# Kernel optimization log

Hardware: AMD Instinct MI355X
Metric: run time of the kernel (lower is better)

The kernel has to match this reference:

```python
import jax, jax.numpy as jnp
import numpy as np

NT, NGRID, NX, HID, NY = 365, 1000, 20, 256, 1


def setup_inputs() -> dict:
    key = jax.random.key(0)
    ks = jax.random.split(key, 10)
    s_in = 1.0 / np.sqrt(NX)
    s_h = 1.0 / np.sqrt(HID)
    inp = {
        "x": jax.random.normal(ks[0], (NT, NGRID, NX), dtype=jnp.float32),
        "wt_ih": jnp.zeros((4 * HID, HID), dtype=jnp.float32),
        "W_in": jax.random.uniform(ks[1], (HID, NX), jnp.float32, -s_in, s_in),
        "b_in": jax.random.uniform(ks[2], (HID,), jnp.float32, -s_in, s_in),
        "W_ih": jax.random.uniform(ks[3], (4 * HID, HID), jnp.float32, -s_h, s_h),
        "W_hh": jax.random.uniform(ks[4], (4 * HID, HID), jnp.float32, -s_h, s_h),
        "b_ih": jax.random.uniform(ks[5], (4 * HID,), jnp.float32, -s_h, s_h),
        "b_hh": jax.random.uniform(ks[6], (4 * HID,), jnp.float32, -s_h, s_h),
        "W_out": jax.random.uniform(ks[7], (NY, HID), jnp.float32, -s_h, s_h),
        "b_out": jax.random.uniform(ks[8], (NY,), jnp.float32, -s_h, s_h),
    }
    return inp


def _lstm_forward(x, W_in, b_in, W_ih, W_hh, b_ih, b_hh, W_out, b_out):
    # linearIn + ReLU: [nt, ngrid, hid]
    x0 = jax.nn.relu(jnp.einsum("tnx,hx->tnh", x, W_in) + b_in)
    # precompute input contribution to gates for all timesteps: [nt, ngrid, 4*hid]
    gx = jnp.einsum("tnh,gh->tng", x0, W_ih) + b_ih + b_hh
    h0 = jnp.zeros((x.shape[1], HID), dtype=x.dtype)
    c0 = jnp.zeros((x.shape[1], HID), dtype=x.dtype)

    def step(carry, gx_t):
        h, c = carry
        gates = gx_t + h @ W_hh.T  # [ngrid, 4*hid]
        i, f, g, o = jnp.split(gates, 4, axis=-1)  # torch LSTMCell gate order
        i = jax.nn.sigmoid(i)
        f = jax.nn.sigmoid(f)
        g = jnp.tanh(g)
        o = jax.nn.sigmoid(o)
        c_new = f * c + i * g
        h_new = o * jnp.tanh(c_new)
        return (h_new, c_new), h_new

    _, hs = jax.lax.scan(step, (h0, c0), gx)  # hs: [nt, ngrid, hid]
    return jnp.einsum("tnh,yh->tny", hs, W_out) + b_out


def reference(x, wt_ih, W_in, b_in, W_ih, W_hh, b_ih, b_hh, W_out, b_out):
    # wt_ih only perturbs weights in training mode (and is zero here); eval-mode math:
    return _lstm_forward(x, W_in, b_in, W_ih, W_hh, b_ih, b_hh, W_out, b_out)
```

## Files before the change

### kernel.cpp

```cpp
#include <hip/hip_runtime.h>
#include <hip/hip_fp16.h>

#define NT    365
#define NGRID 1000
#define NXI   20
#define HID   256
#define GATES 1024
#define MROWS 365000
#define MBLK  5704
#define MPAD  (MBLK * 64)
#define NCL   63
#define CPTS  16
#define HX_TOT ((size_t)NT * NCL * 1024)
#define HX_ZERO ((size_t)NCL * 1024)

typedef _Float16 half8 __attribute__((ext_vector_type(8)));
typedef float floatx4 __attribute__((ext_vector_type(4)));
typedef unsigned long long u64;

#define SENT 0xFFFFFFFFFFFFFFFFull

__device__ _Float16 g_gx[(size_t)MPAD * GATES];
__device__ _Float16 g_wif[64 * 8 * 512];
__device__ _Float16 g_whf[2 * 32 * 8 * 64 * 8];
__device__ u64 g_hx[HX_TOT];

__device__ __forceinline__ float fsig(float x) {
  return __fdividef(1.f, 1.f + __expf(-x));
}
__device__ __forceinline__ float ftanh(float x) {
  return 1.f - __fdividef(2.f, __expf(2.f * x) + 1.f);
}

__global__ __launch_bounds__(256) void init_kernel(float* __restrict__ y) {
  const size_t i = (size_t)blockIdx.x * 256 + threadIdx.x;
  const size_t j = i * 2;
  if (j < HX_TOT)     g_hx[j]     = (j < HX_ZERO)     ? 0ull : SENT;
  if (j + 1 < HX_TOT) g_hx[j + 1] = (j + 1 < HX_ZERO) ? 0ull : SENT;
  if (i < MROWS) y[i] = 0.f;
}

__global__ __launch_bounds__(256) void pack_wf_kernel(
    const float* __restrict__ W_ih, const float* __restrict__ W_hh) {
  const int gid = blockIdx.x * 256 + threadIdx.x;
  const float* src;
  _Float16* dst;
  int n, k0, lane;
  if (gid < 32768) {
    const int tile = gid >> 9;
    const int ks   = (gid >> 6) & 7;
    lane = gid & 63;
    n  = tile * 16 + (lane & 15);
    k0 = ks * 32 + (lane >> 4) * 8;
    src = W_ih + n * HID + k0;
    dst = g_wif + ((size_t)(tile * 8 + ks) * 64 + lane) * 8;
  } else {
    const int rem = gid - 32768;
    const int b2  = rem >> 14;
    const int lt  = (rem >> 9) & 31;
    const int ks  = (rem >> 6) & 7;
    lane = rem & 63;
    const int nt = (lt >> 3) * 16 + b2 * 8 + (lt & 7);
    n  = nt * 16 + (lane & 15);
    k0 = ks * 32 + (lane >> 4) * 8;
    src = W_hh + n * HID + k0;
    dst = g_whf + ((size_t)((b2 * 32 + lt) * 8 + ks) * 64 + lane) * 8;
  }
  const float4 a = *(const float4*)(src);
  const float4 b = *(const float4*)(src + 4);
  half8 h;
  h[0] = (_Float16)a.x; h[1] = (_Float16)a.y; h[2] = (_Float16)a.z; h[3] = (_Float16)a.w;
  h[4] = (_Float16)b.x; h[5] = (_Float16)b.y; h[6] = (_Float16)b.z; h[7] = (_Float16)b.w;
  *(half8*)dst = h;
}

__global__ __launch_bounds__(256, 2) void gx_kernel(
    const float* __restrict__ x, const float* __restrict__ W_in,
    const float* __restrict__ b_in, const float* __restrict__ b_ih,
    const float* __restrict__ b_hh) {
  __shared__ float s_x[64 * NXI];
  __shared__ _Float16 s_x0[64 * 264];
  __shared__ _Float16 s_out[64 * 264];

  const int tid  = threadIdx.x;
  const int lane = tid & 63;
  const int w    = tid >> 6;
  const int m0   = blockIdx.x * 64;

  #pragma unroll
  for (int i = 0; i < 5; ++i) {
    const int idx = i * 256 + tid;
    size_t g = (size_t)m0 * NXI + idx;
    const size_t gmax = (size_t)MROWS * NXI - 1;
    if (g > gmax) g = gmax;
    s_x[idx] = x[g];
  }
  float wv[NXI];
  #pragma unroll
  for (int k = 0; k < NXI; ++k) wv[k] = W_in[tid * NXI + k];
  const float bv = b_in[tid];
  __syncthreads();

  for (int r = 0; r < 64; ++r) {
    float acc = bv;
    #pragma unroll
    for (int qq = 0; qq < 5; ++qq) {
      const float4 xa = *(const float4*)&s_x[r * NXI + qq * 4];
      acc += xa.x * wv[qq * 4 + 0] + xa.y * wv[qq * 4 + 1] +
             xa.z * wv[qq * 4 + 2] + xa.w * wv[qq * 4 + 3];
    }
    s_x0[r * 264 + tid] = (_Float16)fmaxf(acc, 0.f);
  }
  __syncthreads();

  for (int ng = 0; ng < 4; ++ng) {
    floatx4 acc[4][4];
    #pragma unroll
    for (int mi = 0; mi < 4; ++mi)
      #pragma unroll
      for (int ni = 0; ni < 4; ++ni) acc[mi][ni] = (floatx4){0.f, 0.f, 0.f, 0.f};

    #pragma unroll
    for (int ks = 0; ks < 8; ++ks) {
      half8 a[4], bfr[4];
      #pragma unroll
      for (int mi = 0; mi < 4; ++mi)
        a[mi] = *(const half8*)&s_x0[(mi * 16 + (lane & 15)) * 264 + ks * 32 + (lane >> 4) * 8];
      #pragma unroll
      for (int ni = 0; ni < 4; ++ni) {
        const int nt = ng * 16 + w * 4 + ni;
        bfr[ni] = *(const half8*)(g_wif + ((size_t)(nt * 8 + ks) * 64 + lane) * 8);
      }
      #pragma unroll
      for (int mi = 0; mi < 4; ++mi)
        #pragma unroll
        for (int ni = 0; ni < 4; ++ni)
          acc[mi][ni] = __builtin_amdgcn_mfma_f32_16x16x32_f16(a[mi], bfr[ni], acc[mi][ni], 0, 0, 0);
    }

    #pragma unroll
    for (int ni = 0; ni < 4; ++ni) {
      const int g = ng * 256 + (w * 4 + ni) * 16 + (lane & 15);
      const float bias = b_ih[g] + b_hh[g];
      const int colw = (w * 4 + ni) * 16 + (lane & 15);
      #pragma unroll
      for (int mi = 0; mi < 4; ++mi)
        #pragma unroll
        for (int r = 0; r < 4; ++r)
          s_out[(mi * 16 + (lane >> 4) * 4 + r) * 264 + colw] = (_Float16)(acc[mi][ni][r] + bias);
    }
    __syncthreads();

    #pragma unroll
    for (int i = 0; i < 8; ++i) {
      const int cid = i * 256 + tid;
      const int row = cid >> 5;
      const int c8  = (cid & 31) * 8;
      const half8 v = *(const half8*)&s_out[row * 264 + c8];
      const int phi = ((c8 >> 7) & 1) * 512 + ng * 128 + (c8 & 127);
      *(half8*)(g_gx + (size_t)(m0 + row) * GATES + phi) = v;
    }
    __syncthreads();
  }
}

__global__ __launch_bounds__(256, 1) void rec_kernel(
    const float* __restrict__ W_out, const float* __restrict__ b_out,
    float* __restrict__ y) {
  __shared__ float s_g[4 * 16 * 132];
  __shared__ u64   s_h[2][1024];

  const int tid = threadIdx.x;
  const int l   = tid & 63;
  const int w   = tid >> 6;
  const int c   = blockIdx.x >> 1;
  const int b   = blockIdx.x & 1;
  const int pt  = l & 15;
  const int jg  = l >> 4;

  half8 wf[8][8];
  #pragma unroll
  for (int slot = 0; slot < 8; ++slot) {
    const int lt = (slot >> 1) * 8 + 2 * w + (slot & 1);
    #pragma unroll
    for (int kk = 0; kk < 4; ++kk) {
      wf[slot][kk] = *(const half8*)(g_whf +
          ((size_t)((b * 32 + lt) * 8 + (b * 4 + kk)) * 64 + l) * 8);
      wf[slot][4 + kk] = *(const half8*)(g_whf +
          ((size_t)((b * 32 + lt) * 8 + ((1 - b) * 4 + kk)) * 64 + l) * 8);
    }
  }

  float cs[8];
  float wo[8];
  #pragma unroll
  for (int j = 0; j < 8; ++j) {
    cs[j] = 0.f;
    wo[j] = W_out[b * 128 + 32 * w + jg * 8 + j];
  }
  const float bo_eff = (b == 0 && w == 0) ? b_out[0] : 0.f;
  const int n_pt  = c * CPTS + pt;
  const int rn_pt = (n_pt < NGRID) ? n_pt : (NGRID - 1);
  const int peer0 = (1 - b) * 4;

  for (int i = tid; i < 1024; i += 256) s_h[0][i] = 0ull;
  __syncthreads();

  for (int t = 0; t < NT; ++t) {
    const int cur = t & 1, nxt = cur ^ 1;

    half8 gxr[4];
    {
      const _Float16* gsrc = g_gx + ((size_t)t * NGRID + rn_pt) * GATES
                           + b * 512 + 32 * w + jg * 8;
      #pragma unroll
      for (int off = 0; off < 4; ++off)
        gxr[off] = *(const half8*)(gsrc + off * 128);
    }

    const u64* hsrc = g_hx + ((size_t)t * NCL + c) * 1024;
    u64 pv[8];
    #pragma unroll
    for (int kk = 0; kk < 4; ++kk) {
      pv[2 * kk]     = __hip_atomic_load(hsrc +       (peer0 + kk) * 64 + l,
                                         __ATOMIC_RELAXED, __HIP_MEMORY_SCOPE_AGENT);
      pv[2 * kk + 1] = __hip_atomic_load(hsrc + 512 + (peer0 + kk) * 64 + l,
                                         __ATOMIC_RELAXED, __HIP_MEMORY_SCOPE_AGENT);
    }

    floatx4 acc[8];
    #pragma unroll
    for (int i = 0; i < 8; ++i) acc[i] = (floatx4){0.f, 0.f, 0.f, 0.f};

    #pragma unroll
    for (int kk = 0; kk < 4; ++kk) {
      union { u64 u[2]; half8 h; } af;
      af.u[0] = s_h[cur][kk * 64 + l];
      af.u[1] = s_h[cur][512 + kk * 64 + l];
      #pragma unroll
      for (int i = 0; i < 8; ++i)
        acc[i] = __builtin_amdgcn_mfma_f32_16x16x32_f16(af.h, wf[i][kk], acc[i], 0, 0, 0);
    }

    {
      bool pending = false;
      #pragma unroll
      for (int k = 0; k < 8; ++k) pending |= (pv[k] == SENT);
      int tries = 0;
      while (pending && ++tries < (1 << 18)) {
        pending = false;
        #pragma unroll
        for (int kk = 0; kk < 4; ++kk) {
          if (pv[2 * kk] == SENT)
            pv[2 * kk] = __hip_atomic_load(hsrc + (peer0 + kk) * 64 + l,
                                           __ATOMIC_RELAXED, __HIP_MEMORY_SCOPE_AGENT);
          if (pv[2 * kk + 1] == SENT)
            pv[2 * kk + 1] = __hip_atomic_load(hsrc + 512 + (peer0 + kk) * 64 + l,
                                               __ATOMIC_RELAXED, __HIP_MEMORY_SCOPE_AGENT);
        }
        #pragma unroll
        for (int k = 0; k < 8; ++k) pending |= (pv[k] == SENT);
      }
    }

    #pragma unroll
    for (int kk = 0; kk < 4; ++kk) {
      union { u64 u[2]; half8 h; } af;
      af.u[0] = pv[2 * kk];
      af.u[1] = pv[2 * kk + 1];
      #pragma unroll
      for (int i = 0; i < 8; ++i)
        acc[i] = __builtin_amdgcn_mfma_f32_16x16x32_f16(af.h, wf[i][4 + kk], acc[i], 0, 0, 0);
    }

    #pragma unroll
    for (int slot = 0; slot < 8; ++slot) {
      const int colw = (slot >> 1) * 32 + (slot & 1) * 16 + pt;
      #pragma unroll
      for (int r = 0; r < 4; ++r)
        s_g[w * 2112 + (jg * 4 + r) * 132 + colw] = acc[slot][r];
    }

    {
      const float* gp = &s_g[w * 2112 + pt * 132 + jg * 8];
      union { u64 u[2]; _Float16 h[8]; } pub;
      float yp = 0.f;
      #pragma unroll
      for (int j = 0; j < 8; ++j) {
        const float gi = gp[j]      + (float)gxr[0][j];
        const float gf = gp[32 + j] + (float)gxr[1][j];
        const float gg = gp[64 + j] + (float)gxr[2][j];
        const float go = gp[96 + j] + (float)gxr[3][j];
        const float i_ = fsig(gi);
        const float f_ = fsig(gf);
        const float g_ = ftanh(gg);
        const float o_ = fsig(go);
        cs[j] = f_ * cs[j] + i_ * g_;
        const float h = o_ * ftanh(cs[j]);
        pub.h[j] = (_Float16)h;
        yp += wo[j] * h;
      }
      if (t < NT - 1) {
        u64* dst = g_hx + ((size_t)(t + 1) * NCL + c) * 1024 + (b * 4 + w) * 64 + l;
        __hip_atomic_store(dst,       pub.u[0], __ATOMIC_RELAXED, __HIP_MEMORY_SCOPE_AGENT);
        __hip_atomic_store(dst + 512, pub.u[1], __ATOMIC_RELAXED, __HIP_MEMORY_SCOPE_AGENT);
      }
      s_h[nxt][w * 64 + l]       = pub.u[0];
      s_h[nxt][512 + w * 64 + l] = pub.u[1];
      yp += __shfl_xor(yp, 16);
      yp += __shfl_xor(yp, 32);
      if (jg == 0 && n_pt < NGRID)
        atomicAdd(&y[(size_t)t * NGRID + n_pt], yp + bo_eff);
    }
    __syncthreads();
  }
}

extern "C" void kernel_launch(void* const* d_in, const int* in_sizes, int n_in,
                              void* d_out, int out_size, void* d_ws, size_t ws_size,
                              hipStream_t stream) {
  (void)in_sizes; (void)n_in; (void)out_size; (void)d_ws; (void)ws_size;
  const float* x     = (const float*)d_in[0];
  const float* W_in  = (const float*)d_in[2];
  const float* b_in  = (const float*)d_in[3];
  const float* W_ih  = (const float*)d_in[4];
  const float* W_hh  = (const float*)d_in[5];
  const float* b_ih  = (const float*)d_in[6];
  const float* b_hh  = (const float*)d_in[7];
  const float* W_out = (const float*)d_in[8];
  const float* b_out = (const float*)d_in[9];
  float* y           = (float*)d_out;

  const int init_blocks = (int)((HX_TOT / 2 + 255) / 256);
  hipLaunchKernelGGL(init_kernel, dim3(init_blocks), dim3(256), 0, stream, y);
  hipLaunchKernelGGL(pack_wf_kernel, dim3(256), dim3(256), 0, stream, W_ih, W_hh);
  hipLaunchKernelGGL(gx_kernel, dim3(MBLK), dim3(256), 0, stream,
                     x, W_in, b_in, b_ih, b_hh);
  hipLaunchKernelGGL(rec_kernel, dim3(NCL * 2), dim3(256), 0, stream, W_out, b_out, y);
}
```

Measured before the change: 1.866 ms.

## Prefetch next-step peer h, fold init into gx kernel, lighten barrier

The recurrent kernel now issues the atomic loads of the peer block's hidden state for step t+1 one iteration early, so that latency overlaps with the current step's MFMA and gate work. The init kernel is folded into gx_kernel, which removes one launch. The gx loads become nontemporal, shared h is stored as half8, and the full __syncthreads is replaced by an LDS-only waitcnt plus s_barrier so outstanding global ops are not drained. Prefetched values may still be the sentinel, in which case the existing spin loop reloads them, at the cost of extra registers.

Result: slower. 2.262 ms (+21.3%).

```diff
diff --git a/kernel.cpp b/kernel.cpp
--- a/kernel.cpp
+++ b/kernel.cpp
@@ -30,14 +30,6 @@
 }
 __device__ __forceinline__ float ftanh(float x) {
   return 1.f - __fdividef(2.f, __expf(2.f * x) + 1.f);
-}
-
-__global__ __launch_bounds__(256) void init_kernel(float* __restrict__ y) {
-  const size_t i = (size_t)blockIdx.x * 256 + threadIdx.x;
-  const size_t j = i * 2;
-  if (j < HX_TOT)     g_hx[j]     = (j < HX_ZERO)     ? 0ull : SENT;
-  if (j + 1 < HX_TOT) g_hx[j + 1] = (j + 1 < HX_ZERO) ? 0ull : SENT;
-  if (i < MROWS) y[i] = 0.f;
 }
 
 __global__ __launch_bounds__(256) void pack_wf_kernel(
@@ -77,7 +69,15 @@
 __global__ __launch_bounds__(256, 2) void gx_kernel(
     const float* __restrict__ x, const float* __restrict__ W_in,
     const float* __restrict__ b_in, const float* __restrict__ b_ih,
-    const float* __restrict__ b_hh) {
+    const float* __restrict__ b_hh, float* __restrict__ y) {
+  {
+    const size_t gid = (size_t)blockIdx.x * 256 + threadIdx.x;
+    const size_t TT  = (size_t)MBLK * 256;
+    for (size_t j = gid; j < HX_TOT; j += TT)
+      g_hx[j] = (j < HX_ZERO) ? 0ull : SENT;
+    if (gid < MROWS) y[gid] = 0.f;
+  }
+
   __shared__ float s_x[64 * NXI];
   __shared__ _Float16 s_x0[64 * 264];
   __shared__ _Float16 s_out[64 * 264];
@@ -168,7 +168,7 @@
     const float* __restrict__ W_out, const float* __restrict__ b_out,
     float* __restrict__ y) {
   __shared__ float s_g[4 * 16 * 132];
-  __shared__ u64   s_h[2][1024];
+  __shared__ half8 s_h[2][256];
 
   const int tid = threadIdx.x;
   const int l   = tid & 63;
@@ -203,11 +203,25 @@
   const int rn_pt = (n_pt < NGRID) ? n_pt : (NGRID - 1);
   const int peer0 = (1 - b) * 4;
 
-  for (int i = tid; i < 1024; i += 256) s_h[0][i] = 0ull;
+  ((u64*)&s_h[0][0])[tid]       = 0ull;
+  ((u64*)&s_h[0][0])[256 + tid] = 0ull;
+
+  u64 pv[8];
+  {
+    const u64* h0 = g_hx + (size_t)c * 1024;
+    #pragma unroll
+    for (int kk = 0; kk < 4; ++kk) {
+      pv[2 * kk]     = __hip_atomic_load(h0 +       (peer0 + kk) * 64 + l,
+                                         __ATOMIC_RELAXED, __HIP_MEMORY_SCOPE_AGENT);
+      pv[2 * kk + 1] = __hip_atomic_load(h0 + 512 + (peer0 + kk) * 64 + l,
+                                         __ATOMIC_RELAXED, __HIP_MEMORY_SCOPE_AGENT);
+    }
+  }
   __syncthreads();
 
   for (int t = 0; t < NT; ++t) {
     const int cur = t & 1, nxt = cur ^ 1;
+    const bool hasnext = (t + 1 < NT);
 
     half8 gxr[4];
     {
@@ -215,34 +229,35 @@
                            + b * 512 + 32 * w + jg * 8;
       #pragma unroll
       for (int off = 0; off < 4; ++off)
-        gxr[off] = *(const half8*)(gsrc + off * 128);
-    }
-
-    const u64* hsrc = g_hx + ((size_t)t * NCL + c) * 1024;
-    u64 pv[8];
+        gxr[off] = __builtin_nontemporal_load((const half8*)(gsrc + off * 128));
+    }
+
+    u64 pf[8];
+    if (hasnext) {
+      const u64* hnxt = g_hx + ((size_t)(t + 1) * NCL + c) * 1024;
+      #pragma unroll
+      for (int kk = 0; kk < 4; ++kk) {
+        pf[2 * kk]     = __hip_atomic_load(hnxt +       (peer0 + kk) * 64 + l,
+                                           __ATOMIC_RELAXED, __HIP_MEMORY_SCOPE_AGENT);
+        pf[2 * kk + 1] = __hip_atomic_load(hnxt + 512 + (peer0 + kk) * 64 + l,
+                                           __ATOMIC_RELAXED, __HIP_MEMORY_SCOPE_AGENT);
+      }
+    }
+
+    floatx4 acc[8];
+    #pragma unroll
+    for (int i = 0; i < 8; ++i) acc[i] = (floatx4){0.f, 0.f, 0.f, 0.f};
+
     #pragma unroll
     for (int kk = 0; kk < 4; ++kk) {
-      pv[2 * kk]     = __hip_atomic_load(hsrc +       (peer0 + kk) * 64 + l,
-                                         __ATOMIC_RELAXED, __HIP_MEMORY_SCOPE_AGENT);
-      pv[2 * kk + 1] = __hip_atomic_load(hsrc + 512 + (peer0 + kk) * 64 + l,
-                                         __ATOMIC_RELAXED, __HIP_MEMORY_SCOPE_AGENT);
-    }
-
-    floatx4 acc[8];
-    #pragma unroll
-    for (int i = 0; i < 8; ++i) acc[i] = (floatx4){0.f, 0.f, 0.f, 0.f};
-
-    #pragma unroll
-    for (int kk = 0; kk < 4; ++kk) {
-      union { u64 u[2]; half8 h; } af;
-      af.u[0] = s_h[cur][kk * 64 + l];
-      af.u[1] = s_h[cur][512 + kk * 64 + l];
+      const half8 af = s_h[cur][kk * 64 + l];
       #pragma unroll
       for (int i = 0; i < 8; ++i)
-        acc[i] = __builtin_amdgcn_mfma_f32_16x16x32_f16(af.h, wf[i][kk], acc[i], 0, 0, 0);
+        acc[i] = __builtin_amdgcn_mfma_f32_16x16x32_f16(af, wf[i][kk], acc[i], 0, 0, 0);
     }
 
     {
+      const u64* hsrc = g_hx + ((size_t)t * NCL + c) * 1024;
       bool pending = false;
       #pragma unroll
       for (int k = 0; k < 8; ++k) pending |= (pv[k] == SENT);
@@ -283,7 +298,7 @@
 
     {
       const float* gp = &s_g[w * 2112 + pt * 132 + jg * 8];
-      union { u64 u[2]; _Float16 h[8]; } pub;
+      union { u64 u[2]; half8 h8; _Float16 h[8]; } pub;
       float yp = 0.f;
       #pragma unroll
       for (int j = 0; j < 8; ++j) {
@@ -300,19 +315,25 @@
         pub.h[j] = (_Float16)h;
         yp += wo[j] * h;
       }
-      if (t < NT - 1) {
+      if (hasnext) {
         u64* dst = g_hx + ((size_t)(t + 1) * NCL + c) * 1024 + (b * 4 + w) * 64 + l;
         __hip_atomic_store(dst,       pub.u[0], __ATOMIC_RELAXED, __HIP_MEMORY_SCOPE_AGENT);
         __hip_atomic_store(dst + 512, pub.u[1], __ATOMIC_RELAXED, __HIP_MEMORY_SCOPE_AGENT);
       }
-      s_h[nxt][w * 64 + l]       = pub.u[0];
-      s_h[nxt][512 + w * 64 + l] = pub.u[1];
+      s_h[nxt][w * 64 + l] = pub.h8;
       yp += __shfl_xor(yp, 16);
       yp += __shfl_xor(yp, 32);
       if (jg == 0 && n_pt < NGRID)
         atomicAdd(&y[(size_t)t * NGRID + n_pt], yp + bo_eff);
     }
-    __syncthreads();
+
+    if (hasnext) {
+      #pragma unroll
+      for (int k = 0; k < 8; ++k) pv[k] = pf[k];
+    }
+
+    asm volatile("s_waitcnt lgkmcnt(0)" ::: "memory");
+    __builtin_amdgcn_s_barrier();
   }
 }
 
@@ -331,10 +352,8 @@
   const float* b_out = (const float*)d_in[9];
   float* y           = (float*)d_out;
 
-  const int init_blocks = (int)((HX_TOT / 2 + 255) / 256);
-  hipLaunchKernelGGL(init_kernel, dim3(init_blocks), dim3(256), 0, stream, y);
   hipLaunchKernelGGL(pack_wf_kernel, dim3(256), dim3(256), 0, stream, W_ih, W_hh);
   hipLaunchKernelGGL(gx_kernel, dim3(MBLK), dim3(256), 0, stream,
-                     x, W_in, b_in, b_ih, b_hh);
+                     x, W_in, b_in, b_ih, b_hh, y);
   hipLaunchKernelGGL(rec_kernel, dim3(NCL * 2), dim3(256), 0, stream, W_out, b_out, y);
 }
```

## Replace per-step atomicAdd output reduction with LDS sum and cross-block flag exchange

Applied to the files above, without the earlier changes.

Instead of every wave atomically adding its partial output projection into y each timestep, the partials are reduced in shared memory per block. The odd-b block publishes its sum through a sentinel-initialized global slot, and the even-b block polls for it two steps later and writes the final y value with a plain store. This removes eight global atomics per grid point per step and the y zero-init, but adds a delayed spin-wait on the critical recurrent loop and extra shared-memory traffic.

Measured after the change: 1.924 ms. +3.1%, slower.

```diff
diff --git a/kernel.cpp b/kernel.cpp
--- a/kernel.cpp
+++ b/kernel.cpp
@@ -13,6 +13,7 @@
 #define CPTS  16
 #define HX_TOT ((size_t)NT * NCL * 1024)
 #define HX_ZERO ((size_t)NCL * 1024)
+#define YX_TOT ((size_t)NT * NCL * 16)
 
 typedef _Float16 half8 __attribute__((ext_vector_type(8)));
 typedef float floatx4 __attribute__((ext_vector_type(4)));
@@ -24,6 +25,7 @@
 __device__ _Float16 g_wif[64 * 8 * 512];
 __device__ _Float16 g_whf[2 * 32 * 8 * 64 * 8];
 __device__ u64 g_hx[HX_TOT];
+__device__ u64 g_yx[YX_TOT];
 
 __device__ __forceinline__ float fsig(float x) {
   return __fdividef(1.f, 1.f + __expf(-x));
@@ -32,12 +34,12 @@
   return 1.f - __fdividef(2.f, __expf(2.f * x) + 1.f);
 }
 
-__global__ __launch_bounds__(256) void init_kernel(float* __restrict__ y) {
+__global__ __launch_bounds__(256) void init_kernel() {
   const size_t i = (size_t)blockIdx.x * 256 + threadIdx.x;
   const size_t j = i * 2;
   if (j < HX_TOT)     g_hx[j]     = (j < HX_ZERO)     ? 0ull : SENT;
   if (j + 1 < HX_TOT) g_hx[j + 1] = (j + 1 < HX_ZERO) ? 0ull : SENT;
-  if (i < MROWS) y[i] = 0.f;
+  if (i < YX_TOT) g_yx[i] = SENT;
 }
 
 __global__ __launch_bounds__(256) void pack_wf_kernel(
@@ -169,6 +171,7 @@
     float* __restrict__ y) {
   __shared__ float s_g[4 * 16 * 132];
   __shared__ u64   s_h[2][1024];
+  __shared__ float s_y[2][4][16];
 
   const int tid = threadIdx.x;
   const int l   = tid & 63;
@@ -198,16 +201,32 @@
     cs[j] = 0.f;
     wo[j] = W_out[b * 128 + 32 * w + jg * 8 + j];
   }
-  const float bo_eff = (b == 0 && w == 0) ? b_out[0] : 0.f;
+  const float bo = b_out[0];
   const int n_pt  = c * CPTS + pt;
   const int rn_pt = (n_pt < NGRID) ? n_pt : (NGRID - 1);
   const int peer0 = (1 - b) * 4;
+  const bool ylane = (w == 0) && (jg == 0);
+  float yo = 0.f;
 
   for (int i = tid; i < 1024; i += 256) s_h[0][i] = 0ull;
   __syncthreads();
 
   for (int t = 0; t < NT; ++t) {
     const int cur = t & 1, nxt = cur ^ 1;
+
+    float own4 = 0.f;
+    u64 ypk = 0;
+    if (ylane && t >= 1) {
+      own4 = s_y[nxt][0][pt] + s_y[nxt][1][pt] +
+             s_y[nxt][2][pt] + s_y[nxt][3][pt];
+      if (b)
+        __hip_atomic_store(&g_yx[((size_t)(t - 1) * NCL + c) * 16 + pt],
+                           (u64)__float_as_uint(own4),
+                           __ATOMIC_RELAXED, __HIP_MEMORY_SCOPE_AGENT);
+    }
+    if (ylane && !b && t >= 2)
+      ypk = __hip_atomic_load(&g_yx[((size_t)(t - 2) * NCL + c) * 16 + pt],
+                              __ATOMIC_RELAXED, __HIP_MEMORY_SCOPE_AGENT);
 
     half8 gxr[4];
     {
@@ -280,6 +299,17 @@
       for (int r = 0; r < 4; ++r)
         s_g[w * 2112 + (jg * 4 + r) * 132 + colw] = acc[slot][r];
     }
+
+    if (ylane && !b && t >= 2) {
+      int ytr = 0;
+      while (ypk == SENT && ++ytr < (1 << 18))
+        ypk = __hip_atomic_load(&g_yx[((size_t)(t - 2) * NCL + c) * 16 + pt],
+                                __ATOMIC_RELAXED, __HIP_MEMORY_SCOPE_AGENT);
+      if (n_pt < NGRID)
+        y[(size_t)(t - 2) * NGRID + n_pt] =
+            yo + __uint_as_float((unsigned)ypk) + bo;
+    }
+    if (ylane && !b && t >= 1) yo = own4;
 
     {
       const float* gp = &s_g[w * 2112 + pt * 132 + jg * 8];
@@ -309,10 +339,33 @@
       s_h[nxt][512 + w * 64 + l] = pub.u[1];
       yp += __shfl_xor(yp, 16);
       yp += __shfl_xor(yp, 32);
-      if (jg == 0 && n_pt < NGRID)
-        atomicAdd(&y[(size_t)t * NGRID + n_pt], yp + bo_eff);
+      if (jg == 0) s_y[cur][w][pt] = yp;
     }
     __syncthreads();
+  }
+
+  if (ylane) {
+    const int par = (NT - 1) & 1;
+    const float own4 = s_y[par][0][pt] + s_y[par][1][pt] +
+                       s_y[par][2][pt] + s_y[par][3][pt];
+    if (b) {
+      __hip_atomic_store(&g_yx[((size_t)(NT - 1) * NCL + c) * 16 + pt],
+                         (u64)__float_as_uint(own4),
+                         __ATOMIC_RELAXED, __HIP_MEMORY_SCOPE_AGENT);
+    } else {
+      u64 v = SENT; int tr = 0;
+      while (v == SENT && ++tr < (1 << 20))
+        v = __hip_atomic_load(&g_yx[((size_t)(NT - 2) * NCL + c) * 16 + pt],
+                              __ATOMIC_RELAXED, __HIP_MEMORY_SCOPE_AGENT);
+      if (n_pt < NGRID)
+        y[(size_t)(NT - 2) * NGRID + n_pt] = yo + __uint_as_float((unsigned)v) + bo;
+      v = SENT; tr = 0;
+      while (v == SENT && ++tr < (1 << 20))
+        v = __hip_atomic_load(&g_yx[((size_t)(NT - 1) * NCL + c) * 16 + pt],
+                              __ATOMIC_RELAXED, __HIP_MEMORY_SCOPE_AGENT);
+      if (n_pt < NGRID)
+        y[(size_t)(NT - 1) * NGRID + n_pt] = own4 + __uint_as_float((unsigned)v) + bo;
+    }
   }
 }
 
@@ -332,7 +385,7 @@
   float* y           = (float*)d_out;
 
   const int init_blocks = (int)((HX_TOT / 2 + 255) / 256);
-  hipLaunchKernelGGL(init_kernel, dim3(init_blocks), dim3(256), 0, stream, y);
+  hipLaunchKernelGGL(init_kernel, dim3(init_blocks), dim3(256), 0, stream);
   hipLaunchKernelGGL(pack_wf_kernel, dim3(256), dim3(256), 0, stream, W_ih, W_hh);
   hipLaunchKernelGGL(gx_kernel, dim3(MBLK), dim3(256), 0, stream,
                      x, W_in, b_in, b_ih, b_hh);
```

## Prefetch next-step peer hidden state and gate inputs during current step

Applied to the files above, without the earlier changes.

Moves the per-step loads of the peer block's hidden-state fragment and the precomputed gate inputs one iteration ahead, issuing them after the current step's spin-wait so their latency overlaps the second MFMA half and the activation math. The full __syncthreads is replaced by an LDS-only waitcnt plus a raw s_barrier, so the block no longer waits on outstanding global loads and stores at each step. The prefetched peer values are often still sentinels, and the existing retry loop reloads them. It adds register pressure and relies on relaxed atomic ordering for correctness.

After: 2.224 ms. 1.19x slower.

```diff
diff --git a/kernel.cpp b/kernel.cpp
--- a/kernel.cpp
+++ b/kernel.cpp
@@ -204,29 +204,31 @@
   const int peer0 = (1 - b) * 4;
 
   for (int i = tid; i < 1024; i += 256) s_h[0][i] = 0ull;
+
+  u64 pv[8];
+  {
+    const u64* h0 = g_hx + (size_t)c * 1024;
+    #pragma unroll
+    for (int kk = 0; kk < 4; ++kk) {
+      pv[2 * kk]     = __hip_atomic_load(h0 +       (peer0 + kk) * 64 + l,
+                                         __ATOMIC_RELAXED, __HIP_MEMORY_SCOPE_AGENT);
+      pv[2 * kk + 1] = __hip_atomic_load(h0 + 512 + (peer0 + kk) * 64 + l,
+                                         __ATOMIC_RELAXED, __HIP_MEMORY_SCOPE_AGENT);
+    }
+  }
+  half8 gxr[4];
+  {
+    const _Float16* gsrc = g_gx + (size_t)rn_pt * GATES + b * 512 + 32 * w + jg * 8;
+    #pragma unroll
+    for (int off = 0; off < 4; ++off)
+      gxr[off] = *(const half8*)(gsrc + off * 128);
+  }
   __syncthreads();
 
   for (int t = 0; t < NT; ++t) {
     const int cur = t & 1, nxt = cur ^ 1;
-
-    half8 gxr[4];
-    {
-      const _Float16* gsrc = g_gx + ((size_t)t * NGRID + rn_pt) * GATES
-                           + b * 512 + 32 * w + jg * 8;
-      #pragma unroll
-      for (int off = 0; off < 4; ++off)
-        gxr[off] = *(const half8*)(gsrc + off * 128);
-    }
-
+    const bool hasnext = (t + 1 < NT);
     const u64* hsrc = g_hx + ((size_t)t * NCL + c) * 1024;
-    u64 pv[8];
-    #pragma unroll
-    for (int kk = 0; kk < 4; ++kk) {
-      pv[2 * kk]     = __hip_atomic_load(hsrc +       (peer0 + kk) * 64 + l,
-                                         __ATOMIC_RELAXED, __HIP_MEMORY_SCOPE_AGENT);
-      pv[2 * kk + 1] = __hip_atomic_load(hsrc + 512 + (peer0 + kk) * 64 + l,
-                                         __ATOMIC_RELAXED, __HIP_MEMORY_SCOPE_AGENT);
-    }
 
     floatx4 acc[8];
     #pragma unroll
@@ -263,6 +265,24 @@
       }
     }
 
+    u64 tn[8];
+    half8 gn[4];
+    if (hasnext) {
+      const u64* hnxt = g_hx + ((size_t)(t + 1) * NCL + c) * 1024;
+      #pragma unroll
+      for (int kk = 0; kk < 4; ++kk) {
+        tn[2 * kk]     = __hip_atomic_load(hnxt +       (peer0 + kk) * 64 + l,
+                                           __ATOMIC_RELAXED, __HIP_MEMORY_SCOPE_AGENT);
+        tn[2 * kk + 1] = __hip_atomic_load(hnxt + 512 + (peer0 + kk) * 64 + l,
+                                           __ATOMIC_RELAXED, __HIP_MEMORY_SCOPE_AGENT);
+      }
+      const _Float16* gsrc = g_gx + ((size_t)(t + 1) * NGRID + rn_pt) * GATES
+                           + b * 512 + 32 * w + jg * 8;
+      #pragma unroll
+      for (int off = 0; off < 4; ++off)
+        gn[off] = *(const half8*)(gsrc + off * 128);
+    }
+
     #pragma unroll
     for (int kk = 0; kk < 4; ++kk) {
       union { u64 u[2]; half8 h; } af;
@@ -300,7 +320,7 @@
         pub.h[j] = (_Float16)h;
         yp += wo[j] * h;
       }
-      if (t < NT - 1) {
+      if (hasnext) {
         u64* dst = g_hx + ((size_t)(t + 1) * NCL + c) * 1024 + (b * 4 + w) * 64 + l;
         __hip_atomic_store(dst,       pub.u[0], __ATOMIC_RELAXED, __HIP_MEMORY_SCOPE_AGENT);
         __hip_atomic_store(dst + 512, pub.u[1], __ATOMIC_RELAXED, __HIP_MEMORY_SCOPE_AGENT);
@@ -312,7 +332,17 @@
       if (jg == 0 && n_pt < NGRID)
         atomicAdd(&y[(size_t)t * NGRID + n_pt], yp + bo_eff);
     }
-    __syncthreads();
+
+    if (hasnext) {
+      #pragma unroll
+      for (int k = 0; k < 8; ++k) pv[k] = tn[k];
+      #pragma unroll
+      for (int off = 0; off < 4; ++off) gxr[off] = gn[off];
+    }
+
+    asm volatile("s_waitcnt lgkmcnt(0)" ::: "memory");
+    __builtin_amdgcn_s_barrier();
+    __builtin_amdgcn_sched_barrier(0);
   }
 }
 
```
